# Kernel optimization log

Hardware: AMD Instinct MI355X
Metric: run time of the kernel (lower is better)

Reference implementation:

```python
import jax, jax.numpy as jnp
import numpy as np


def setup_inputs() -> dict:
    key = jax.random.key(0)
    ks = jax.random.split(key, 7)
    B, N, K, D = 256, 50, 12, 128
    return {
        "batch_size": B,
        "itm_emb": jax.random.normal(ks[0], (B, N, D), jnp.float32),
        "ave_sess_itms_emb": jax.random.normal(ks[1], (B, N, D), jnp.float32),
        "glob_adj_itm_embs": jax.random.normal(ks[2], (B, N, K, D), jnp.float32),
        "glob_adj_wgt_embs": jax.random.normal(ks[3], (B, N, K), jnp.float32),
        "w1": jax.random.normal(ks[4], (D + 1, D), jnp.float32) * 0.1,
        "w2": jax.random.normal(ks[5], (D, 1), jnp.float32) * 0.1,
        "w3": jax.random.normal(ks[6], (2 * D, D), jnp.float32) * 0.1,
    }


def reference(batch_size, itm_emb, ave_sess_itms_emb, glob_adj_itm_embs,
              glob_adj_wgt_embs, w1, w2, w3):
    D = itm_emb.shape[-1]
    # [B,N,1,D] * [B,N,K,D] -> [B,N,K,D]; concat weight -> [B,N,K,D+1]
    alpha = ave_sess_itms_emb[:, :, None, :] * glob_adj_itm_embs
    alpha = jnp.concatenate([alpha, glob_adj_wgt_embs[..., None]], axis=-1)
    alpha = jnp.einsum('bnkc,cd->bnkd', alpha, w1)          # [B,N,K,D]
    alpha = jax.nn.leaky_relu(alpha, negative_slope=0.2)
    alpha = jnp.einsum('bnkd,do->bnk', alpha, w2)           # [B,N,K]
    alpha = jax.nn.softmax(alpha, axis=-1)[..., None]       # [B,N,K,1]
    att = jnp.sum(alpha * glob_adj_itm_embs, axis=-2)       # [B,N,D]
    g = jnp.concatenate([itm_emb, att], axis=-1)            # [B,N,2D]
    # dropout with p=0.0 / eval mode is identity
    g = jnp.einsum('bnc,cd->bnd', g, w3)
    g = g.reshape(batch_size, -1, D)
    return jax.nn.relu(g)
```

## Files before the change

kernel.cpp:

```cpp
#include <hip/hip_runtime.h>

#define DD 128
#define KADJ 12
#define BN_TOTAL 12800

typedef float f32x4 __attribute__((ext_vector_type(4)));
typedef float f32x2 __attribute__((ext_vector_type(2)));
typedef __bf16 bf16x8 __attribute__((ext_vector_type(8)));
typedef __bf16 bf16x2 __attribute__((ext_vector_type(2)));
typedef unsigned int u32;

__device__ __forceinline__ bf16x8 cvt8(f32x4 a, f32x4 b) {
    bf16x8 r;
    r[0] = (__bf16)a[0]; r[1] = (__bf16)a[1]; r[2] = (__bf16)a[2]; r[3] = (__bf16)a[3];
    r[4] = (__bf16)b[0]; r[5] = (__bf16)b[1]; r[6] = (__bf16)b[2]; r[7] = (__bf16)b[3];
    return r;
}

__device__ __forceinline__ bf16x8 mul8(bf16x8 a, bf16x8 b) {
    bf16x8 r;
    #pragma unroll
    for (int i = 0; i < 8; ++i) r[i] = (__bf16)((float)a[i] * (float)b[i]);
    return r;
}

__global__ void k_prep(const float* __restrict__ w1, const float* __restrict__ w3,
                       __bf16* __restrict__ w1f, __bf16* __restrict__ w3f) {
    int idx = blockIdx.x * 256 + threadIdx.x;
    int lane = (idx >> 3) & 63, e = idx & 7;
    int l = lane & 15, gg = lane >> 4;
    if (idx < 16384) {
        int fi = idx >> 9, n = fi >> 2, ks = fi & 3;
        int k = ks * 32 + gg * 8 + e;
        w1f[idx] = (__bf16)w1[k * DD + n * 16 + l];
    } else {
        int j = idx - 16384;
        int fi = j >> 9, n = fi >> 3, ks = fi & 7;
        int k = ks * 32 + gg * 8 + e;
        w3f[j] = (__bf16)w3[k * DD + n * 16 + l];
    }
}

__launch_bounds__(512, 4)
__global__ void k_att(const float* __restrict__ ave, const float* __restrict__ adj,
                      const float* __restrict__ wgt, const float* __restrict__ w1,
                      const float* __restrict__ w2, const __bf16* __restrict__ w1f,
                      float* __restrict__ att_out) {
    __shared__ unsigned char lds[32768 + 8 * (3072 + 272)];
    const int t = threadIdx.x;
    const int lane = t & 63;
    const int w = t >> 6;
    const int l = lane & 15, g = lane >> 4;
    const int bn = blockIdx.x * 8 + w;
    const size_t abase = (size_t)bn * (KADJ * DD);

    __bf16* w1s = (__bf16*)lds;
    unsigned char* adjb = lds + 32768 + w * 3072;
    unsigned char* aveb = lds + 32768 + 8 * 3072 + w * 272;

    {
        const f32x4* src = (const f32x4*)w1f;
        f32x4* dst = (f32x4*)w1s;
        #pragma unroll
        for (int p = 0; p < 4; ++p) dst[p * 512 + t] = src[p * 512 + t];
    }
    #pragma unroll
    for (int i = 0; i < 3; ++i) {
        int row = i * 4 + g;
        const float* gs = adj + abase + (size_t)row * DD + l * 8;
        f32x4 v0 = __builtin_nontemporal_load(reinterpret_cast<const f32x4*>(gs));
        f32x4 v1 = __builtin_nontemporal_load(reinterpret_cast<const f32x4*>(gs + 4));
        *reinterpret_cast<bf16x8*>(adjb + row * 256 + ((l ^ row) << 4)) = cvt8(v0, v1);
    }
    {
        f32x2 v = *reinterpret_cast<const f32x2*>(ave + (size_t)bn * DD + lane * 2);
        bf16x2 bv; bv[0] = (__bf16)v[0]; bv[1] = (__bf16)v[1];
        *reinterpret_cast<bf16x2*>(aveb + lane * 4) = bv;
    }
    __syncthreads();

    float w1r[8], w2v[8];
    #pragma unroll
    for (int n = 0; n < 8; ++n) {
        w1r[n] = w1[128 * DD + n * 16 + l];
        w2v[n] = w2[n * 16 + l];
    }

    const int l2 = l < KADJ ? l : KADJ - 1;
    f32x4 acc[8];
    #pragma unroll
    for (int n = 0; n < 8; ++n) acc[n] = f32x4{0.f, 0.f, 0.f, 0.f};
    #pragma unroll
    for (int ks = 0; ks < 4; ++ks) {
        bf16x8 adjf = *reinterpret_cast<const bf16x8*>(
            adjb + l2 * 256 + (((ks * 4 + g) ^ l2) << 4));
        bf16x8 avef = *reinterpret_cast<const bf16x8*>(aveb + ks * 64 + g * 16);
        bf16x8 af = mul8(adjf, avef);
        const __bf16* bp = w1s + ((size_t)ks * 64 + lane) * 8;
        #pragma unroll
        for (int n = 0; n < 8; ++n) {
            bf16x8 bfr = *reinterpret_cast<const bf16x8*>(bp + (size_t)n * 2048);
            acc[n] = __builtin_amdgcn_mfma_f32_16x16x32_bf16(af, bfr, acc[n], 0, 0, 0);
        }
    }

    float wv[4];
    #pragma unroll
    for (int j = 0; j < 4; ++j) {
        int r = g * 4 + j;
        wv[j] = (r < KADJ) ? wgt[(size_t)bn * KADJ + r] : 0.f;
    }
    float p[4] = {0.f, 0.f, 0.f, 0.f};
    #pragma unroll
    for (int n = 0; n < 8; ++n) {
        #pragma unroll
        for (int j = 0; j < 4; ++j) {
            float h = fmaf(wv[j], w1r[n], acc[n][j]);
            h = h > 0.f ? h : 0.2f * h;
            p[j] = fmaf(h, w2v[n], p[j]);
        }
    }
    #pragma unroll
    for (int j = 0; j < 4; ++j) {
        p[j] += __shfl_xor(p[j], 1, 64);
        p[j] += __shfl_xor(p[j], 2, 64);
        p[j] += __shfl_xor(p[j], 4, 64);
        p[j] += __shfl_xor(p[j], 8, 64);
        if (g == 3) p[j] = -1e30f;
    }

    float q0[4], q1[4], q2[4];
    #pragma unroll
    for (int j = 0; j < 4; ++j) {
        q0[j] = __shfl_xor(p[j], 16, 64);
        q1[j] = __shfl_xor(p[j], 32, 64);
        q2[j] = __shfl_xor(q1[j], 16, 64);
    }
    float mx = -1e30f;
    #pragma unroll
    for (int j = 0; j < 4; ++j)
        mx = fmaxf(mx, fmaxf(fmaxf(p[j], q0[j]), fmaxf(q1[j], q2[j])));
    float ssum = 0.f;
    #pragma unroll
    for (int j = 0; j < 4; ++j) {
        ssum += __expf(p[j] - mx);  ssum += __expf(q0[j] - mx);
        ssum += __expf(q1[j] - mx); ssum += __expf(q2[j] - mx);
    }
    float inv = 1.f / ssum;

    float a0 = 0.f, a1 = 0.f;
    #pragma unroll
    for (int k = 0; k < KADJ; ++k) {
        int d = (k >> 2) ^ g, j = k & 3;
        float sv = (d == 0) ? p[j] : (d == 1) ? q0[j] : (d == 2) ? q1[j] : q2[j];
        float alpha = __expf(sv - mx) * inv;
        u32 pk = *reinterpret_cast<const u32*>(
            adjb + k * 256 + ((((lane >> 2) ^ k)) << 4) + (lane & 3) * 4);
        float e0 = __builtin_bit_cast(float, pk << 16);
        float e1 = __builtin_bit_cast(float, pk & 0xFFFF0000u);
        a0 = fmaf(alpha, e0, a0);
        a1 = fmaf(alpha, e1, a1);
    }
    *reinterpret_cast<f32x2*>(att_out + (size_t)bn * DD + lane * 2) = f32x2{a0, a1};
}

__launch_bounds__(256)
__global__ void k_out(const float* __restrict__ itm, const float* att,
                      const __bf16* __restrict__ w3f, float* outp) {
    const int t = threadIdx.x;
    const int lane = t & 63;
    const int w = t >> 6;
    const int l = lane & 15, g = lane >> 4;
    const int R0 = blockIdx.x * 64 + w * 16;
    const int row = R0 + l;

    bf16x8 afr[8];
    const float* ip = itm + (size_t)row * DD;
    #pragma unroll
    for (int s = 0; s < 4; ++s) {
        int c = s * 32 + g * 8;
        f32x4 a0 = *reinterpret_cast<const f32x4*>(ip + c);
        f32x4 a1 = *reinterpret_cast<const f32x4*>(ip + c + 4);
        afr[s] = cvt8(a0, a1);
    }
    const float* ap = att + (size_t)row * DD;
    #pragma unroll
    for (int s = 0; s < 4; ++s) {
        int c = s * 32 + g * 8;
        f32x4 a0 = *reinterpret_cast<const f32x4*>(ap + c);
        f32x4 a1 = *reinterpret_cast<const f32x4*>(ap + c + 4);
        afr[4 + s] = cvt8(a0, a1);
    }

    f32x4 acc[8];
    #pragma unroll
    for (int n = 0; n < 8; ++n) acc[n] = f32x4{0.f, 0.f, 0.f, 0.f};
    #pragma unroll
    for (int s = 0; s < 8; ++s) {
        const __bf16* bp = w3f + ((size_t)s * 64 + lane) * 8;
        #pragma unroll
        for (int n = 0; n < 8; ++n) {
            bf16x8 bfr = *reinterpret_cast<const bf16x8*>(bp + (size_t)n * 4096);
            acc[n] = __builtin_amdgcn_mfma_f32_16x16x32_bf16(afr[s], bfr, acc[n], 0, 0, 0);
        }
    }

    #pragma unroll
    for (int n = 0; n < 8; ++n) {
        #pragma unroll
        for (int j = 0; j < 4; ++j)
            outp[(size_t)(R0 + g * 4 + j) * DD + n * 16 + l] = fmaxf(acc[n][j], 0.f);
    }
}

extern "C" void kernel_launch(void* const* d_in, const int* in_sizes, int n_in,
                              void* d_out, int out_size, void* d_ws, size_t ws_size,
                              hipStream_t stream) {
    const float* itm = (const float*)d_in[1];
    const float* ave = (const float*)d_in[2];
    const float* adj = (const float*)d_in[3];
    const float* wgt = (const float*)d_in[4];
    const float* w1  = (const float*)d_in[5];
    const float* w2  = (const float*)d_in[6];
    const float* w3  = (const float*)d_in[7];
    float* outp = (float*)d_out;

    __bf16* w1f = (__bf16*)d_ws;
    __bf16* w3f = (__bf16*)((char*)d_ws + 32 * 1024);

    k_prep<<<dim3(192), dim3(256), 0, stream>>>(w1, w3, w1f, w3f);
    k_att<<<dim3(BN_TOTAL / 8), dim3(512), 0, stream>>>(ave, adj, wgt, w1, w2, w1f, outp);
    k_out<<<dim3(BN_TOTAL / 64), dim3(256), 0, stream>>>(itm, outp, w3f, outp);
}
```

Before: 51.94 us.

## Make attention waves persistent over 8 rows with register-resident W1 and prefetch

```diff
diff --git a/kernel.cpp b/kernel.cpp
--- a/kernel.cpp
+++ b/kernel.cpp
@@ -41,43 +41,28 @@
     }
 }
 
-__launch_bounds__(512, 4)
+__launch_bounds__(256, 2)
 __global__ void k_att(const float* __restrict__ ave, const float* __restrict__ adj,
                       const float* __restrict__ wgt, const float* __restrict__ w1,
                       const float* __restrict__ w2, const __bf16* __restrict__ w1f,
                       float* __restrict__ att_out) {
-    __shared__ unsigned char lds[32768 + 8 * (3072 + 272)];
+    __shared__ unsigned char lds[4 * 3344];
     const int t = threadIdx.x;
     const int lane = t & 63;
     const int w = t >> 6;
     const int l = lane & 15, g = lane >> 4;
-    const int bn = blockIdx.x * 8 + w;
-    const size_t abase = (size_t)bn * (KADJ * DD);
-
-    __bf16* w1s = (__bf16*)lds;
-    unsigned char* adjb = lds + 32768 + w * 3072;
-    unsigned char* aveb = lds + 32768 + 8 * 3072 + w * 272;
-
-    {
-        const f32x4* src = (const f32x4*)w1f;
-        f32x4* dst = (f32x4*)w1s;
-        #pragma unroll
-        for (int p = 0; p < 4; ++p) dst[p * 512 + t] = src[p * 512 + t];
-    }
-    #pragma unroll
-    for (int i = 0; i < 3; ++i) {
-        int row = i * 4 + g;
-        const float* gs = adj + abase + (size_t)row * DD + l * 8;
-        f32x4 v0 = __builtin_nontemporal_load(reinterpret_cast<const f32x4*>(gs));
-        f32x4 v1 = __builtin_nontemporal_load(reinterpret_cast<const f32x4*>(gs + 4));
-        *reinterpret_cast<bf16x8*>(adjb + row * 256 + ((l ^ row) << 4)) = cvt8(v0, v1);
-    }
-    {
-        f32x2 v = *reinterpret_cast<const f32x2*>(ave + (size_t)bn * DD + lane * 2);
-        bf16x2 bv; bv[0] = (__bf16)v[0]; bv[1] = (__bf16)v[1];
-        *reinterpret_cast<bf16x2*>(aveb + lane * 4) = bv;
-    }
-    __syncthreads();
+    const int bn0 = (blockIdx.x * 4 + w) * 8;
+
+    unsigned char* adjb = lds + w * 3344;
+    unsigned char* aveb = adjb + 3072;
+
+    bf16x8 bfr[4][8];
+    #pragma unroll
+    for (int ks = 0; ks < 4; ++ks)
+        #pragma unroll
+        for (int n = 0; n < 8; ++n)
+            bfr[ks][n] = *reinterpret_cast<const bf16x8*>(
+                w1f + ((size_t)(n * 4 + ks) * 512 + lane * 8));
 
     float w1r[8], w2v[8];
     #pragma unroll
@@ -86,82 +71,110 @@
         w2v[n] = w2[n * 16 + l];
     }
 
-    const int l2 = l < KADJ ? l : KADJ - 1;
-    f32x4 acc[8];
-    #pragma unroll
-    for (int n = 0; n < 8; ++n) acc[n] = f32x4{0.f, 0.f, 0.f, 0.f};
-    #pragma unroll
-    for (int ks = 0; ks < 4; ++ks) {
-        bf16x8 adjf = *reinterpret_cast<const bf16x8*>(
-            adjb + l2 * 256 + (((ks * 4 + g) ^ l2) << 4));
-        bf16x8 avef = *reinterpret_cast<const bf16x8*>(aveb + ks * 64 + g * 16);
-        bf16x8 af = mul8(adjf, avef);
-        const __bf16* bp = w1s + ((size_t)ks * 64 + lane) * 8;
+    f32x4 pa[6]; f32x2 pv; f32x4 pw;
+    #define ISSUE(BN) do {                                                        \
+        const float* gs_ = adj + (size_t)(BN) * (KADJ * DD);                      \
+        _Pragma("unroll")                                                         \
+        for (int i_ = 0; i_ < 3; ++i_) {                                          \
+            int row_ = i_ * 4 + g;                                                \
+            pa[2*i_]   = __builtin_nontemporal_load(                              \
+                reinterpret_cast<const f32x4*>(gs_ + row_ * DD + l * 8));         \
+            pa[2*i_+1] = __builtin_nontemporal_load(                              \
+                reinterpret_cast<const f32x4*>(gs_ + row_ * DD + l * 8 + 4));     \
+        }                                                                         \
+        pv = *reinterpret_cast<const f32x2*>(ave + (size_t)(BN) * DD + lane * 2); \
+        pw = (g < 3) ? *reinterpret_cast<const f32x4*>(wgt + (size_t)(BN) * KADJ + g * 4) \
+                     : f32x4{0.f, 0.f, 0.f, 0.f};                                 \
+    } while (0)
+
+    ISSUE(bn0);
+
+    for (int it = 0; it < 8; ++it) {
+        const int bn = bn0 + it;
+
+        #pragma unroll
+        for (int i = 0; i < 3; ++i) {
+            int row = i * 4 + g;
+            *reinterpret_cast<bf16x8*>(adjb + row * 256 + ((l ^ row) << 4)) =
+                cvt8(pa[2 * i], pa[2 * i + 1]);
+        }
+        {
+            bf16x2 bv; bv[0] = (__bf16)pv[0]; bv[1] = (__bf16)pv[1];
+            *reinterpret_cast<bf16x2*>(aveb + lane * 4) = bv;
+        }
+        f32x4 wvv = pw;
+
+        if (it < 7) ISSUE(bn + 1);
+
+        const int l2 = l < KADJ ? l : KADJ - 1;
+        f32x4 acc[8];
+        #pragma unroll
+        for (int n = 0; n < 8; ++n) acc[n] = f32x4{0.f, 0.f, 0.f, 0.f};
+        #pragma unroll
+        for (int ks = 0; ks < 4; ++ks) {
+            bf16x8 adjf = *reinterpret_cast<const bf16x8*>(
+                adjb + l2 * 256 + (((ks * 4 + g) ^ l2) << 4));
+            bf16x8 avef = *reinterpret_cast<const bf16x8*>(aveb + ks * 64 + g * 16);
+            bf16x8 af = mul8(adjf, avef);
+            #pragma unroll
+            for (int n = 0; n < 8; ++n)
+                acc[n] = __builtin_amdgcn_mfma_f32_16x16x32_bf16(af, bfr[ks][n], acc[n], 0, 0, 0);
+        }
+
+        float p[4] = {0.f, 0.f, 0.f, 0.f};
         #pragma unroll
         for (int n = 0; n < 8; ++n) {
-            bf16x8 bfr = *reinterpret_cast<const bf16x8*>(bp + (size_t)n * 2048);
-            acc[n] = __builtin_amdgcn_mfma_f32_16x16x32_bf16(af, bfr, acc[n], 0, 0, 0);
-        }
-    }
-
-    float wv[4];
-    #pragma unroll
-    for (int j = 0; j < 4; ++j) {
-        int r = g * 4 + j;
-        wv[j] = (r < KADJ) ? wgt[(size_t)bn * KADJ + r] : 0.f;
-    }
-    float p[4] = {0.f, 0.f, 0.f, 0.f};
-    #pragma unroll
-    for (int n = 0; n < 8; ++n) {
+            #pragma unroll
+            for (int j = 0; j < 4; ++j) {
+                float h = fmaf(wvv[j], w1r[n], acc[n][j]);
+                h = h > 0.f ? h : 0.2f * h;
+                p[j] = fmaf(h, w2v[n], p[j]);
+            }
+        }
         #pragma unroll
         for (int j = 0; j < 4; ++j) {
-            float h = fmaf(wv[j], w1r[n], acc[n][j]);
-            h = h > 0.f ? h : 0.2f * h;
-            p[j] = fmaf(h, w2v[n], p[j]);
-        }
-    }
-    #pragma unroll
-    for (int j = 0; j < 4; ++j) {
-        p[j] += __shfl_xor(p[j], 1, 64);
-        p[j] += __shfl_xor(p[j], 2, 64);
-        p[j] += __shfl_xor(p[j], 4, 64);
-        p[j] += __shfl_xor(p[j], 8, 64);
-        if (g == 3) p[j] = -1e30f;
-    }
-
-    float q0[4], q1[4], q2[4];
-    #pragma unroll
-    for (int j = 0; j < 4; ++j) {
-        q0[j] = __shfl_xor(p[j], 16, 64);
-        q1[j] = __shfl_xor(p[j], 32, 64);
-        q2[j] = __shfl_xor(q1[j], 16, 64);
-    }
-    float mx = -1e30f;
-    #pragma unroll
-    for (int j = 0; j < 4; ++j)
-        mx = fmaxf(mx, fmaxf(fmaxf(p[j], q0[j]), fmaxf(q1[j], q2[j])));
-    float ssum = 0.f;
-    #pragma unroll
-    for (int j = 0; j < 4; ++j) {
-        ssum += __expf(p[j] - mx);  ssum += __expf(q0[j] - mx);
-        ssum += __expf(q1[j] - mx); ssum += __expf(q2[j] - mx);
-    }
-    float inv = 1.f / ssum;
-
-    float a0 = 0.f, a1 = 0.f;
-    #pragma unroll
-    for (int k = 0; k < KADJ; ++k) {
-        int d = (k >> 2) ^ g, j = k & 3;
-        float sv = (d == 0) ? p[j] : (d == 1) ? q0[j] : (d == 2) ? q1[j] : q2[j];
-        float alpha = __expf(sv - mx) * inv;
-        u32 pk = *reinterpret_cast<const u32*>(
-            adjb + k * 256 + ((((lane >> 2) ^ k)) << 4) + (lane & 3) * 4);
-        float e0 = __builtin_bit_cast(float, pk << 16);
-        float e1 = __builtin_bit_cast(float, pk & 0xFFFF0000u);
-        a0 = fmaf(alpha, e0, a0);
-        a1 = fmaf(alpha, e1, a1);
-    }
-    *reinterpret_cast<f32x2*>(att_out + (size_t)bn * DD + lane * 2) = f32x2{a0, a1};
+            p[j] += __shfl_xor(p[j], 1, 64);
+            p[j] += __shfl_xor(p[j], 2, 64);
+            p[j] += __shfl_xor(p[j], 4, 64);
+            p[j] += __shfl_xor(p[j], 8, 64);
+            if (g == 3) p[j] = -1e30f;
+        }
+
+        float q0[4], q1[4], q2[4];
+        #pragma unroll
+        for (int j = 0; j < 4; ++j) {
+            q0[j] = __shfl_xor(p[j], 16, 64);
+            q1[j] = __shfl_xor(p[j], 32, 64);
+            q2[j] = __shfl_xor(q1[j], 16, 64);
+        }
+        float mx = -1e30f;
+        #pragma unroll
+        for (int j = 0; j < 4; ++j)
+            mx = fmaxf(mx, fmaxf(fmaxf(p[j], q0[j]), fmaxf(q1[j], q2[j])));
+        float ssum = 0.f;
+        #pragma unroll
+        for (int j = 0; j < 4; ++j) {
+            ssum += __expf(p[j] - mx);  ssum += __expf(q0[j] - mx);
+            ssum += __expf(q1[j] - mx); ssum += __expf(q2[j] - mx);
+        }
+        float inv = 1.f / ssum;
+
+        float a0 = 0.f, a1 = 0.f;
+        #pragma unroll
+        for (int k = 0; k < KADJ; ++k) {
+            int d = (k >> 2) ^ g, j = k & 3;
+            float sv = (d == 0) ? p[j] : (d == 1) ? q0[j] : (d == 2) ? q1[j] : q2[j];
+            float alpha = __expf(sv - mx) * inv;
+            u32 pk = *reinterpret_cast<const u32*>(
+                adjb + k * 256 + ((((lane >> 2) ^ k)) << 4) + (lane & 3) * 4);
+            float e0 = __builtin_bit_cast(float, pk << 16);
+            float e1 = __builtin_bit_cast(float, pk & 0xFFFF0000u);
+            a0 = fmaf(alpha, e0, a0);
+            a1 = fmaf(alpha, e1, a1);
+        }
+        *reinterpret_cast<f32x2*>(att_out + (size_t)bn * DD + lane * 2) = f32x2{a0, a1};
+    }
+    #undef ISSUE
 }
 
 __launch_bounds__(256)
@@ -229,6 +242,6 @@
     __bf16* w3f = (__bf16*)((char*)d_ws + 32 * 1024);
 
     k_prep<<<dim3(192), dim3(256), 0, stream>>>(w1, w3, w1f, w3f);
-    k_att<<<dim3(BN_TOTAL / 8), dim3(512), 0, stream>>>(ave, adj, wgt, w1, w2, w1f, outp);
+    k_att<<<dim3(BN_TOTAL / 32), dim3(256), 0, stream>>>(ave, adj, wgt, w1, w2, w1f, outp);
     k_out<<<dim3(BN_TOTAL / 64), dim3(256), 0, stream>>>(itm, outp, w3f, outp);
 }
```

New measurement: 63.16 us. 1.22x slower.

## Load W1 fragments into registers and share adjacency staging block-wide

Applied to the files above, without the earlier changes.

```diff
diff --git a/kernel.cpp b/kernel.cpp
--- a/kernel.cpp
+++ b/kernel.cpp
@@ -46,122 +46,112 @@
                       const float* __restrict__ wgt, const float* __restrict__ w1,
                       const float* __restrict__ w2, const __bf16* __restrict__ w1f,
                       float* __restrict__ att_out) {
-    __shared__ unsigned char lds[32768 + 8 * (3072 + 272)];
+    __shared__ unsigned char lds[96 * 256 + 8 * 272 + 96 * 4];
+    unsigned char* adjb = lds;
+    unsigned char* aveb = lds + 96 * 256;
+    float* sco = (float*)(lds + 96 * 256 + 8 * 272);
+
     const int t = threadIdx.x;
     const int lane = t & 63;
     const int w = t >> 6;
     const int l = lane & 15, g = lane >> 4;
-    const int bn = blockIdx.x * 8 + w;
-    const size_t abase = (size_t)bn * (KADJ * DD);
-
-    __bf16* w1s = (__bf16*)lds;
-    unsigned char* adjb = lds + 32768 + w * 3072;
-    unsigned char* aveb = lds + 32768 + 8 * 3072 + w * 272;
-
-    {
-        const f32x4* src = (const f32x4*)w1f;
-        f32x4* dst = (f32x4*)w1s;
-        #pragma unroll
-        for (int p = 0; p < 4; ++p) dst[p * 512 + t] = src[p * 512 + t];
-    }
+    const int Bn0 = blockIdx.x * 8;
+    const size_t R0 = (size_t)Bn0 * KADJ;
+
+    bf16x8 bfr[4][8];
+    #pragma unroll
+    for (int ks = 0; ks < 4; ++ks)
+        #pragma unroll
+        for (int n = 0; n < 8; ++n)
+            bfr[ks][n] = *reinterpret_cast<const bf16x8*>(
+                w1f + ((size_t)(n * 4 + ks) * 512 + lane * 8));
+
     #pragma unroll
     for (int i = 0; i < 3; ++i) {
-        int row = i * 4 + g;
-        const float* gs = adj + abase + (size_t)row * DD + l * 8;
+        int idx = i * 512 + t;
+        int row = idx >> 4, c8 = idx & 15;
+        const float* gs = adj + (R0 + row) * (size_t)DD + c8 * 8;
         f32x4 v0 = __builtin_nontemporal_load(reinterpret_cast<const f32x4*>(gs));
         f32x4 v1 = __builtin_nontemporal_load(reinterpret_cast<const f32x4*>(gs + 4));
-        *reinterpret_cast<bf16x8*>(adjb + row * 256 + ((l ^ row) << 4)) = cvt8(v0, v1);
+        *reinterpret_cast<bf16x8*>(adjb + row * 256 + ((c8 ^ (row & 15)) << 4)) =
+            cvt8(v0, v1);
     }
     {
-        f32x2 v = *reinterpret_cast<const f32x2*>(ave + (size_t)bn * DD + lane * 2);
+        f32x2 v = *reinterpret_cast<const f32x2*>(ave + (size_t)(Bn0 + w) * DD + lane * 2);
         bf16x2 bv; bv[0] = (__bf16)v[0]; bv[1] = (__bf16)v[1];
-        *reinterpret_cast<bf16x2*>(aveb + lane * 4) = bv;
+        *reinterpret_cast<bf16x2*>(aveb + w * 272 + lane * 4) = bv;
     }
     __syncthreads();
 
-    float w1r[8], w2v[8];
-    #pragma unroll
-    for (int n = 0; n < 8; ++n) {
-        w1r[n] = w1[128 * DD + n * 16 + l];
-        w2v[n] = w2[n * 16 + l];
-    }
-
-    const int l2 = l < KADJ ? l : KADJ - 1;
-    f32x4 acc[8];
-    #pragma unroll
-    for (int n = 0; n < 8; ++n) acc[n] = f32x4{0.f, 0.f, 0.f, 0.f};
-    #pragma unroll
-    for (int ks = 0; ks < 4; ++ks) {
-        bf16x8 adjf = *reinterpret_cast<const bf16x8*>(
-            adjb + l2 * 256 + (((ks * 4 + g) ^ l2) << 4));
-        bf16x8 avef = *reinterpret_cast<const bf16x8*>(aveb + ks * 64 + g * 16);
-        bf16x8 af = mul8(adjf, avef);
-        const __bf16* bp = w1s + ((size_t)ks * 64 + lane) * 8;
+    {
+        const int lr = w * 12 + (l < KADJ ? l : KADJ - 1);
+        f32x4 acc[8];
+        #pragma unroll
+        for (int n = 0; n < 8; ++n) acc[n] = f32x4{0.f, 0.f, 0.f, 0.f};
+        #pragma unroll
+        for (int ks = 0; ks < 4; ++ks) {
+            bf16x8 adjf = *reinterpret_cast<const bf16x8*>(
+                adjb + lr * 256 + (((ks * 4 + g) ^ (lr & 15)) << 4));
+            bf16x8 avef = *reinterpret_cast<const bf16x8*>(
+                aveb + w * 272 + ks * 64 + g * 16);
+            bf16x8 af = mul8(adjf, avef);
+            #pragma unroll
+            for (int n = 0; n < 8; ++n)
+                acc[n] = __builtin_amdgcn_mfma_f32_16x16x32_bf16(af, bfr[ks][n], acc[n], 0, 0, 0);
+        }
+        float wv[4];
+        #pragma unroll
+        for (int j = 0; j < 4; ++j)
+            wv[j] = (g < 3) ? wgt[R0 + (size_t)w * 12 + g * 4 + j] : 0.f;
+        float p[4] = {0.f, 0.f, 0.f, 0.f};
         #pragma unroll
         for (int n = 0; n < 8; ++n) {
-            bf16x8 bfr = *reinterpret_cast<const bf16x8*>(bp + (size_t)n * 2048);
-            acc[n] = __builtin_amdgcn_mfma_f32_16x16x32_bf16(af, bfr, acc[n], 0, 0, 0);
-        }
-    }
-
-    float wv[4];
-    #pragma unroll
-    for (int j = 0; j < 4; ++j) {
-        int r = g * 4 + j;
-        wv[j] = (r < KADJ) ? wgt[(size_t)bn * KADJ + r] : 0.f;
-    }
-    float p[4] = {0.f, 0.f, 0.f, 0.f};
-    #pragma unroll
-    for (int n = 0; n < 8; ++n) {
+            float w1rn = w1[128 * DD + n * 16 + l];
+            float w2vn = w2[n * 16 + l];
+            #pragma unroll
+            for (int j = 0; j < 4; ++j) {
+                float h = fmaf(wv[j], w1rn, acc[n][j]);
+                h = h > 0.f ? h : 0.2f * h;
+                p[j] = fmaf(h, w2vn, p[j]);
+            }
+        }
         #pragma unroll
         for (int j = 0; j < 4; ++j) {
-            float h = fmaf(wv[j], w1r[n], acc[n][j]);
-            h = h > 0.f ? h : 0.2f * h;
-            p[j] = fmaf(h, w2v[n], p[j]);
-        }
-    }
-    #pragma unroll
-    for (int j = 0; j < 4; ++j) {
-        p[j] += __shfl_xor(p[j], 1, 64);
-        p[j] += __shfl_xor(p[j], 2, 64);
-        p[j] += __shfl_xor(p[j], 4, 64);
-        p[j] += __shfl_xor(p[j], 8, 64);
-        if (g == 3) p[j] = -1e30f;
-    }
-
-    float q0[4], q1[4], q2[4];
-    #pragma unroll
-    for (int j = 0; j < 4; ++j) {
-        q0[j] = __shfl_xor(p[j], 16, 64);
-        q1[j] = __shfl_xor(p[j], 32, 64);
-        q2[j] = __shfl_xor(q1[j], 16, 64);
-    }
-    float mx = -1e30f;
-    #pragma unroll
-    for (int j = 0; j < 4; ++j)
-        mx = fmaxf(mx, fmaxf(fmaxf(p[j], q0[j]), fmaxf(q1[j], q2[j])));
-    float ssum = 0.f;
-    #pragma unroll
-    for (int j = 0; j < 4; ++j) {
-        ssum += __expf(p[j] - mx);  ssum += __expf(q0[j] - mx);
-        ssum += __expf(q1[j] - mx); ssum += __expf(q2[j] - mx);
-    }
-    float inv = 1.f / ssum;
-
-    float a0 = 0.f, a1 = 0.f;
-    #pragma unroll
-    for (int k = 0; k < KADJ; ++k) {
-        int d = (k >> 2) ^ g, j = k & 3;
-        float sv = (d == 0) ? p[j] : (d == 1) ? q0[j] : (d == 2) ? q1[j] : q2[j];
-        float alpha = __expf(sv - mx) * inv;
-        u32 pk = *reinterpret_cast<const u32*>(
-            adjb + k * 256 + ((((lane >> 2) ^ k)) << 4) + (lane & 3) * 4);
-        float e0 = __builtin_bit_cast(float, pk << 16);
-        float e1 = __builtin_bit_cast(float, pk & 0xFFFF0000u);
-        a0 = fmaf(alpha, e0, a0);
-        a1 = fmaf(alpha, e1, a1);
-    }
-    *reinterpret_cast<f32x2*>(att_out + (size_t)bn * DD + lane * 2) = f32x2{a0, a1};
+            p[j] += __shfl_xor(p[j], 1, 64);
+            p[j] += __shfl_xor(p[j], 2, 64);
+            p[j] += __shfl_xor(p[j], 4, 64);
+            p[j] += __shfl_xor(p[j], 8, 64);
+        }
+        if (l == 0 && g < 3)
+            *reinterpret_cast<f32x4*>(&sco[w * 12 + g * 4]) =
+                f32x4{p[0], p[1], p[2], p[3]};
+    }
+    __syncthreads();
+
+    {
+        float s[KADJ];
+        float mx = -1e30f;
+        #pragma unroll
+        for (int k = 0; k < KADJ; ++k) { s[k] = sco[w * 12 + k]; mx = fmaxf(mx, s[k]); }
+        float ssum = 0.f;
+        #pragma unroll
+        for (int k = 0; k < KADJ; ++k) { s[k] = __expf(s[k] - mx); ssum += s[k]; }
+        float inv = 1.f / ssum;
+        float a0 = 0.f, a1 = 0.f;
+        #pragma unroll
+        for (int k = 0; k < KADJ; ++k) {
+            int row = w * 12 + k;
+            u32 pk = *reinterpret_cast<const u32*>(
+                adjb + row * 256 + (((lane >> 2) ^ (row & 15)) << 4) + (lane & 3) * 4);
+            float alpha = s[k] * inv;
+            float e0 = __builtin_bit_cast(float, pk << 16);
+            float e1 = __builtin_bit_cast(float, pk & 0xFFFF0000u);
+            a0 = fmaf(alpha, e0, a0);
+            a1 = fmaf(alpha, e1, a1);
+        }
+        *reinterpret_cast<f32x2*>(att_out + (size_t)(Bn0 + w) * DD + lane * 2) =
+            f32x2{a0, a1};
+    }
 }
 
 __launch_bounds__(256)
```

After: 90.03 us. 1.73x slower.
